# Kernel optimization log

Hardware: AMD Instinct MI355X
Metric: run time of the kernel (lower is better)

Reference implementation:

```python
import jax, jax.numpy as jnp
import numpy as np
import math

B, N, F, H = 16, 256, 1024, 16
HD = F // H  # head_dim = 64
NEG = -9e15


def setup_inputs() -> dict:
    key = jax.random.key(0)
    ks = jax.random.split(key, 12)
    s = 0.02
    return {
        "obj_feats": jax.random.normal(ks[0], (B, N, F), jnp.float32),
        "cross_feats": jax.random.normal(ks[1], (B, N, F), jnp.float32),
        "adj_matrix": jax.random.randint(ks[2], (B, N, N), 0, 2, jnp.int32),
        "label_biases_att": jax.random.normal(ks[3], (B, N, N), jnp.float32),
        "Wq": jax.random.normal(ks[4], (F, F), jnp.float32) * s,
        "bq": jnp.zeros((F,), jnp.float32),
        "Wk": jax.random.normal(ks[5], (F, F), jnp.float32) * s,
        "bk": jnp.zeros((F,), jnp.float32),
        "Wv": jax.random.normal(ks[6], (F, F), jnp.float32) * s,
        "bv": jnp.zeros((F,), jnp.float32),
        # grouped 1x1 conv: out=F, groups=H, in_per_group=F -> weight [F, F]
        "Wo": jax.random.normal(ks[7], (F, F), jnp.float32) * s,
        "bo": jnp.zeros((F,), jnp.float32),
    }


def reference(obj_feats, cross_feats, adj_matrix, label_biases_att,
              Wq, bq, Wk, bk, Wv, bv, Wo, bo):
    # projections (torch Linear: x @ W.T + b)
    q = (jnp.einsum('bnf,gf->bng', obj_feats, Wq) + bq).reshape(B, N, H, HD)
    k = (jnp.einsum('bnf,gf->bng', cross_feats, Wk) + bk).reshape(B, N, H, HD)
    v = jnp.einsum('bnf,gf->bng', cross_feats, Wv) + bv          # [B, N, F] (NOT split per head)

    scale = 1.0 / math.sqrt(float(HD))
    att = jnp.einsum('bqhd,bkhd->bqhk', q, k) * scale            # [B, Nq, H, Nk]

    # adjacency mask broadcast over heads + label bias (both indexed [b, q, k])
    mask = (adj_matrix > 0)[:, :, None, :]                       # [B, Nq, 1, Nk]
    att = jnp.where(mask, att, NEG) + label_biases_att[:, :, None, :]

    p = jax.nn.softmax(att, axis=-1)                             # softmax over keys

    # weighted sum against un-split values: [B, Nq, H, Nk] x [B, Nk, F]
    out = jnp.einsum('bqhk,bkf->bqhf', p, v)                     # [B, Nq, H, F]

    # grouped 1x1 conv: group h maps its F input channels -> HD output channels
    Wo_g = Wo.reshape(H, HD, F)
    out = jnp.einsum('bqhf,hdf->bqhd', out, Wo_g) + bo.reshape(H, HD)
    out = out.reshape(B, N, F)

    att_mean = p.sum(axis=2) / H                                 # [B, Nq, Nk]
    return out, att_mean
```

## Files before the change

### kernel.cpp

```cpp
#include <hip/hip_runtime.h>

#define NEGF -9e15f

typedef __attribute__((ext_vector_type(8))) unsigned short u16x8;
typedef __attribute__((ext_vector_type(8))) short          s16x8;
typedef __attribute__((ext_vector_type(4))) float          f32x4;

__device__ __forceinline__ unsigned short f2bf(float x) {
  union { float f; unsigned int u; } c; c.f = x;
  unsigned int r = c.u + 0x7fffu + ((c.u >> 16) & 1u);
  return (unsigned short)(r >> 16);
}
__device__ __forceinline__ float bf2f(unsigned short v) {
  union { float f; unsigned int u; } c; c.u = ((unsigned int)v) << 16;
  return c.f;
}

__device__ __forceinline__ void gload16(const void* g, void* l) {
  __builtin_amdgcn_global_load_lds(
      (const __attribute__((address_space(1))) unsigned int*)g,
      (__attribute__((address_space(3))) unsigned int*)l, 16, 0, 0);
}

__global__ __launch_bounds__(256) void cvt2_bf16(
    const float* __restrict__ a, const float* __restrict__ b,
    unsigned short* __restrict__ oa, unsigned short* __restrict__ ob)
{
  const int bid = blockIdx.x;
  const float* in = (bid < 4096) ? a : b;
  unsigned short* out = (bid < 4096) ? oa : ob;
  const int i = ((bid & 4095) * 256 + threadIdx.x) * 4;
  const float4 v = *(const float4*)(in + i);
  ushort4 o;
  o.x = f2bf(v.x); o.y = f2bf(v.y); o.z = f2bf(v.z); o.w = f2bf(v.w);
  *(ushort4*)(out + i) = o;
}

__global__ __launch_bounds__(256) void prep_w(
    const float* __restrict__ Wq, const float* __restrict__ Wk,
    const float* __restrict__ Wo, const float* __restrict__ Wv,
    unsigned short* __restrict__ Wall, unsigned short* __restrict__ Wo_bf,
    unsigned short* __restrict__ Wvt_bf)
{
  __shared__ float tile[32][33];
  const int bid = blockIdx.x;
  if (bid < 3072) {
    const int i = ((bid & 1023) * 256 + threadIdx.x) * 4;
    const float* in;
    unsigned short* out;
    float sc = 1.f;
    if (bid < 1024)      { in = Wq; out = Wall;           sc = 0.125f; }
    else if (bid < 2048) { in = Wk; out = Wall + 1048576; }
    else                 { in = Wo; out = Wo_bf; }
    const float4 v = *(const float4*)(in + i);
    ushort4 o;
    o.x = f2bf(v.x * sc); o.y = f2bf(v.y * sc);
    o.z = f2bf(v.z * sc); o.w = f2bf(v.w * sc);
    *(ushort4*)(out + i) = o;
  } else {
    const int j = bid - 3072;
    const int bc = (j & 31) * 32, br = (j >> 5) * 32;
    const int tx = threadIdx.x & 31, ty8 = threadIdx.x >> 5;
    #pragma unroll
    for (int jj = 0; jj < 32; jj += 8)
      tile[ty8 + jj][tx] = Wv[(size_t)(br + ty8 + jj) * 1024 + bc + tx];
    __syncthreads();
    #pragma unroll
    for (int jj = 0; jj < 32; jj += 8)
      Wvt_bf[(size_t)(bc + ty8 + jj) * 1024 + br + tx] = f2bf(tile[tx][ty8 + jj]);
  }
}

__global__ __launch_bounds__(256) void prep_bias(
    const float* __restrict__ bq, const float* __restrict__ bk,
    const float* __restrict__ Wo, const float* __restrict__ bv,
    float* __restrict__ ball)
{
  const int bid = blockIdx.x;
  if (bid < 4) {
    const int i = bid * 256 + threadIdx.x;
    ball[i]        = 0.125f * bq[i];
    ball[1024 + i] = bk[i];
  } else {
    const int g    = (bid - 4) * 4 + (threadIdx.x >> 6);
    const int lane = threadIdx.x & 63;
    float acc = 0.f;
    for (int f = lane; f < 1024; f += 64)
      acc = fmaf(Wo[(size_t)g * 1024 + f], bv[f], acc);
    #pragma unroll
    for (int off = 32; off > 0; off >>= 1) acc += __shfl_down(acc, off);
    if (lane == 0) ball[2048 + g] = acc;
  }
}

__global__ __launch_bounds__(256) void mb_prep(
    const int* __restrict__ adj, const float* __restrict__ lab,
    float* __restrict__ mb)
{
  const int i = (blockIdx.x * 256 + threadIdx.x) * 4;
  const int4   a = *(const int4*)(adj + i);
  const float4 l = *(const float4*)(lab + i);
  float4 o;
  o.x = a.x > 0 ? l.x : NEGF;
  o.y = a.y > 0 ? l.y : NEGF;
  o.z = a.z > 0 ? l.z : NEGF;
  o.w = a.w > 0 ? l.w : NEGF;
  *(float4*)(mb + i) = o;
}

__global__ __launch_bounds__(256, 3) void gemm_wov(
    const unsigned short* __restrict__ A,
    const unsigned short* __restrict__ Bw,
    unsigned short* __restrict__ Cout)
{
  __shared__ unsigned short Asm[128 * 64];
  __shared__ unsigned short Bsm[64 * 64];
  const int t = threadIdx.x;
  const int lane = t & 63, w = t >> 6;
  const int wm = w >> 1, wn = w & 1;
  const int bm = blockIdx.y * 128, bn = blockIdx.x * 64;

  const int srow = lane >> 3;
  const int skel = (lane & 7) * 8;
  const int fr = lane & 15, kf = (lane >> 4) * 8;

  f32x4 acc[4][2] = {};

  for (int k0 = 0; k0 < 1024; k0 += 64) {
    if (k0) __syncthreads();
    #pragma unroll
    for (int i = 0; i < 4; ++i) {
      const int c = i * 4 + w;
      const int r = c * 8 + srow;
      gload16(A + (size_t)(bm + r) * 1024 + k0 + skel, &Asm[c * 512]);
    }
    #pragma unroll
    for (int i = 0; i < 2; ++i) {
      const int c = i * 4 + w;
      const int r = c * 8 + srow;
      gload16(Bw + (size_t)(bn + r) * 1024 + k0 + skel, &Bsm[c * 512]);
    }
    __syncthreads();
    #pragma unroll
    for (int kk = 0; kk < 2; ++kk) {
      s16x8 af[4], bf[2];
      #pragma unroll
      for (int fm = 0; fm < 4; ++fm)
        af[fm] = *(const s16x8*)&Asm[(wm * 64 + fm * 16 + fr) * 64 + kk * 32 + kf];
      #pragma unroll
      for (int fn = 0; fn < 2; ++fn)
        bf[fn] = *(const s16x8*)&Bsm[(wn * 32 + fn * 16 + fr) * 64 + kk * 32 + kf];
      #pragma unroll
      for (int fm = 0; fm < 4; ++fm)
        #pragma unroll
        for (int fn = 0; fn < 2; ++fn)
          acc[fm][fn] = __builtin_amdgcn_mfma_f32_16x16x32_bf16(af[fm], bf[fn], acc[fm][fn], 0, 0, 0);
    }
  }

  const int rg = (lane >> 4) * 4;
  #pragma unroll
  for (int fm = 0; fm < 4; ++fm)
    #pragma unroll
    for (int fn = 0; fn < 2; ++fn) {
      const int col = bn + wn * 32 + fn * 16 + fr;
      #pragma unroll
      for (int r = 0; r < 4; ++r) {
        const int row = bm + wm * 64 + fm * 16 + rg + r;
        Cout[(size_t)row * 1024 + col] = f2bf(acc[fm][fn][r]);
      }
    }
}

__global__ __launch_bounds__(256, 3) void gemm_big(
    const unsigned short* __restrict__ objA,
    const unsigned short* __restrict__ crossA,
    const unsigned short* __restrict__ Wall,
    const float* __restrict__ ball,
    unsigned short* __restrict__ Qo,
    unsigned short* __restrict__ Ko,
    unsigned short* __restrict__ VWt)
{
  __shared__ unsigned short Asm[128 * 64];
  __shared__ unsigned short Bsm[128 * 64];
  const int t = threadIdx.x;
  const int w = t >> 6, lane = t & 63;
  const int wm = w >> 1, wn = w & 1;

  const int bid = blockIdx.x;
  const int xcd = bid & 7, j = bid >> 3;
  const int bmi = (xcd >> 1) * 8 + j / 12;
  const int bni = (xcd & 1) * 12 + j % 12;
  const int bm = bmi * 128;
  const int bn = bni * 128;
  const unsigned short* Ag = (bn < 1024) ? objA : crossA;

  const int srow = lane >> 3;
  const int skel = (lane & 7) * 8;
  const int fr = lane & 15, kf = (lane >> 4) * 8;

  f32x4 acc[4][4] = {};

  for (int k0 = 0; k0 < 1024; k0 += 64) {
    if (k0) __syncthreads();
    #pragma unroll
    for (int i = 0; i < 4; ++i) {
      const int c = i * 4 + w;
      const int r = c * 8 + srow;
      gload16(Ag   + (size_t)(bm + r) * 1024 + k0 + skel, &Asm[c * 512]);
      gload16(Wall + (size_t)(bn + r) * 1024 + k0 + skel, &Bsm[c * 512]);
    }
    __syncthreads();
    #pragma unroll
    for (int kk = 0; kk < 2; ++kk) {
      s16x8 af[4], bf[4];
      #pragma unroll
      for (int fm = 0; fm < 4; ++fm)
        af[fm] = *(const s16x8*)&Asm[(wm * 64 + fm * 16 + fr) * 64 + kk * 32 + kf];
      #pragma unroll
      for (int fn = 0; fn < 4; ++fn)
        bf[fn] = *(const s16x8*)&Bsm[(wn * 64 + fn * 16 + fr) * 64 + kk * 32 + kf];
      #pragma unroll
      for (int fm = 0; fm < 4; ++fm)
        #pragma unroll
        for (int fn = 0; fn < 4; ++fn)
          acc[fm][fn] = __builtin_amdgcn_mfma_f32_16x16x32_bf16(af[fm], bf[fn], acc[fm][fn], 0, 0, 0);
    }
  }

  const int rg = (lane >> 4) * 4;
  const int mode = bn >> 10;
  #pragma unroll
  for (int fm = 0; fm < 4; ++fm) {
    #pragma unroll
    for (int fn = 0; fn < 4; ++fn) {
      const int col  = bn + wn * 64 + fn * 16 + fr;
      const int cl   = col & 1023;
      const float bb = ball[col];
      const int row0 = bm + wm * 64 + fm * 16 + rg;
      if (mode == 0) {
        #pragma unroll
        for (int r = 0; r < 4; ++r)
          Qo[(size_t)(row0 + r) * 1024 + cl] = f2bf(acc[fm][fn][r] + bb);
      } else if (mode == 1) {
        #pragma unroll
        for (int r = 0; r < 4; ++r)
          Ko[(size_t)(row0 + r) * 1024 + cl] = f2bf(acc[fm][fn][r] + bb);
      } else {
        const int bidx = row0 >> 8, tok = row0 & 255;
        ushort4 u;
        u.x = f2bf(acc[fm][fn][0] + bb);
        u.y = f2bf(acc[fm][fn][1] + bb);
        u.z = f2bf(acc[fm][fn][2] + bb);
        u.w = f2bf(acc[fm][fn][3] + bb);
        *(ushort4*)(VWt + ((size_t)bidx * 1024 + cl) * 256 + tok) = u;
      }
    }
  }
}

__global__ __launch_bounds__(256, 2) void attn_mfma(
    const unsigned short* __restrict__ Qg,
    const unsigned short* __restrict__ Kg,
    const unsigned short* __restrict__ VWt,
    const float* __restrict__ mb,
    const float* __restrict__ bo,
    float* __restrict__ outp, unsigned short* __restrict__ Pb)
{
  const int t = threadIdx.x;
  const int w = t >> 6, lane = t & 63;
  const int fr = lane & 15, grp = lane >> 4;
  const int bid = blockIdx.x;
  const int xcd = bid & 7, i = bid >> 3;
  const int h   = i & 15;
  const int bqt = xcd * 8 + (i >> 4);
  const int b   = bqt >> 2;
  const int qt  = bqt & 3;
  const int q0 = qt * 64 + w * 16;

  __shared__ __align__(16) unsigned short Ks[256 * 64];
  __shared__ __align__(16) unsigned short VWs[64 * 256];

  {
    const unsigned short* kb = Kg + (size_t)(b * 256) * 1024 + h * 64;
    const int colb = (lane & 7) * 16;
    #pragma unroll
    for (int c = 0; c < 8; ++c) {
      const int row = c * 32 + w * 8 + (lane >> 3);
      const int sb  = colb ^ ((row & 7) << 4);
      gload16(kb + (size_t)row * 1024 + (sb >> 1), (char*)Ks + c * 4096 + w * 1024);
    }
  }
  {
    const unsigned short* vwb = VWt + (size_t)(b * 16 + h) * 16384;
    const int xb = (lane & 31) * 16;
    #pragma unroll
    for (int c = 0; c < 8; ++c) {
      const int row = c * 8 + w * 2 + (lane >> 5);
      const int sb  = xb ^ ((row & 7) << 4);
      gload16(vwb + row * 256 + (sb >> 1), (char*)VWs + c * 4096 + w * 1024);
    }
  }

  const unsigned short* qp = Qg + ((size_t)(b * 256 + q0 + fr)) * 1024 + h * 64 + grp * 8;
  const s16x8 qf0 = *(const s16x8*)qp;
  const s16x8 qf1 = *(const s16x8*)(qp + 32);

  __syncthreads();

  const float* mbp = mb + ((size_t)(b * 256 + q0 + fr)) * 256 + grp * 4;
  const int colA = (grp * 16) ^ ((fr & 7) << 4);

  f32x4 s[16];
  #pragma unroll
  for (int nf = 0; nf < 16; ++nf) s[nf] = (f32x4){0.f, 0.f, 0.f, 0.f};

  s16x8 kA[8], kB[8];
  float4 mA[4], mB[4];
  float mx = -3e38f;

#define LOADB(KF, MF, nb)                                                    \
  { _Pragma("unroll") for (int i2 = 0; i2 < 4; ++i2) {                       \
      const char* rp = (const char*)Ks + (((nb)*4 + i2) * 16 + fr) * 128;    \
      KF[2*i2]   = *(const s16x8*)(rp + colA);                               \
      KF[2*i2+1] = *(const s16x8*)(rp + (colA ^ 64));                        \
      MF[i2]     = *(const float4*)(mbp + ((nb)*4 + i2) * 16); } }
#define MFMAB(KF, nb)                                                        \
  { _Pragma("unroll") for (int i2 = 0; i2 < 4; ++i2) {                       \
      s[(nb)*4+i2] = __builtin_amdgcn_mfma_f32_16x16x32_bf16(KF[2*i2],   qf0, s[(nb)*4+i2], 0, 0, 0); \
      s[(nb)*4+i2] = __builtin_amdgcn_mfma_f32_16x16x32_bf16(KF[2*i2+1], qf1, s[(nb)*4+i2], 0, 0, 0); } }
#define MASKB(MF, nb)                                                        \
  { _Pragma("unroll") for (int i2 = 0; i2 < 4; ++i2) {                       \
      _Pragma("unroll") for (int r = 0; r < 4; ++r) {                        \
        const float m = ((const float*)&MF[i2])[r];                          \
        const float v = (m > -1e14f) ? s[(nb)*4+i2][r] + m : m;              \
        s[(nb)*4+i2][r] = v; mx = fmaxf(mx, v); } } }

  LOADB(kA, mA, 0); LOADB(kB, mB, 1); MFMAB(kA, 0);
  MASKB(mA, 0);     LOADB(kA, mA, 2); MFMAB(kB, 1);
  MASKB(mB, 1);     LOADB(kB, mB, 3); MFMAB(kA, 2);
  MASKB(mA, 2);     LOADB(kA, mA, 4); MFMAB(kB, 3);
  MASKB(mB, 3);     LOADB(kB, mB, 5); MFMAB(kA, 4);
  MASKB(mA, 4);     LOADB(kA, mA, 6); MFMAB(kB, 5);
  MASKB(mB, 5);     LOADB(kB, mB, 7); MFMAB(kA, 6);
  MASKB(mA, 6);     MFMAB(kB, 7);     MASKB(mB, 7);
#undef LOADB
#undef MFMAB
#undef MASKB

  mx = fmaxf(mx, __shfl_xor(mx, 16));
  mx = fmaxf(mx, __shfl_xor(mx, 32));
  float sm = 0.f;
  #pragma unroll
  for (int nf = 0; nf < 16; ++nf)
    #pragma unroll
    for (int r = 0; r < 4; ++r) {
      const float e = __expf(s[nf][r] - mx);
      s[nf][r] = e;
      sm += e;
    }
  sm += __shfl_xor(sm, 16);
  sm += __shfl_xor(sm, 32);
  const float inv = 1.f / sm;

  uint2 u2[16];
  #pragma unroll
  for (int nf = 0; nf < 16; ++nf) {
    const unsigned lo = (unsigned)f2bf(s[nf][0] * inv) | ((unsigned)f2bf(s[nf][1] * inv) << 16);
    const unsigned hi = (unsigned)f2bf(s[nf][2] * inv) | ((unsigned)f2bf(s[nf][3] * inv) << 16);
    u2[nf] = make_uint2(lo, hi);
  }

  unsigned short* prow = Pb + (((size_t)(b * 16 + h)) * 256 + q0 + fr) * 256 + grp * 4;
  #pragma unroll
  for (int nf = 0; nf < 16; ++nf)
    *(uint2*)(prow + nf * 16) = u2[nf];

  f32x4 o[4];
  #pragma unroll
  for (int nf = 0; nf < 4; ++nf) o[nf] = (f32x4){0.f, 0.f, 0.f, 0.f};
  const int srcA = fr + ((grp & 1) << 5);
  const int srcB = srcA + 16;
  const int swz  = (fr & 7) << 4;
  const bool hiSel = (grp & 2);
  #pragma unroll
  for (int ks = 0; ks < 8; ++ks) {
    const int aLx = __shfl((int)u2[2 * ks].x,     srcA, 64);
    const int aLy = __shfl((int)u2[2 * ks].y,     srcA, 64);
    const int bLx = __shfl((int)u2[2 * ks].x,     srcB, 64);
    const int bLy = __shfl((int)u2[2 * ks].y,     srcB, 64);
    const int aHx = __shfl((int)u2[2 * ks + 1].x, srcA, 64);
    const int aHy = __shfl((int)u2[2 * ks + 1].y, srcA, 64);
    const int bHx = __shfl((int)u2[2 * ks + 1].x, srcB, 64);
    const int bHy = __shfl((int)u2[2 * ks + 1].y, srcB, 64);
    union { int4 i; s16x8 v; } pf;
    pf.i = hiSel ? make_int4(aHx, aHy, bHx, bHy) : make_int4(aLx, aLy, bLx, bLy);
    const int cb = (ks * 64 + grp * 16) ^ swz;
    #pragma unroll
    for (int nf = 0; nf < 4; ++nf) {
      const s16x8 vf = *(const s16x8*)((const char*)VWs + (nf * 16 + fr) * 512 + cb);
      o[nf] = __builtin_amdgcn_mfma_f32_16x16x32_bf16(pf.v, vf, o[nf], 0, 0, 0);
    }
  }

  #pragma unroll
  for (int nf = 0; nf < 4; ++nf) {
    const float bb = bo[h * 64 + nf * 16 + fr];
    #pragma unroll
    for (int r = 0; r < 4; ++r)
      outp[((size_t)b * 256 + q0 + grp * 4 + r) * 1024 + h * 64 + nf * 16 + fr]
          = o[nf][r] + bb;
  }
}

__global__ __launch_bounds__(256) void attm_reduce(
    const unsigned short* __restrict__ Pb, float* __restrict__ attm)
{
  const size_t idx = (size_t)blockIdx.x * 256 + threadIdx.x;
  const int    k8  = (int)(idx & 31);
  const size_t bq  = idx >> 5;
  const int    b   = (int)(bq >> 8);
  const int    q   = (int)(bq & 255);
  float s[8] = {};
  const unsigned short* base = Pb + (size_t)b * 1048576 + (size_t)q * 256 + k8 * 8;
  #pragma unroll
  for (int hh = 0; hh < 16; ++hh) {
    const u16x8 p = *(const u16x8*)(base + (size_t)hh * 65536);
    #pragma unroll
    for (int j = 0; j < 8; ++j) s[j] += bf2f(p[j]);
  }
  float* dst = attm + bq * 256 + k8 * 8;
  float4 r0, r1;
  r0.x = s[0] * 0.0625f; r0.y = s[1] * 0.0625f; r0.z = s[2] * 0.0625f; r0.w = s[3] * 0.0625f;
  r1.x = s[4] * 0.0625f; r1.y = s[5] * 0.0625f; r1.z = s[6] * 0.0625f; r1.w = s[7] * 0.0625f;
  *(float4*)dst = r0;
  *(float4*)(dst + 4) = r1;
}

extern "C" void kernel_launch(void* const* d_in, const int* in_sizes, int n_in,
                              void* d_out, int out_size, void* d_ws, size_t ws_size,
                              hipStream_t stream)
{
  const float* obj   = (const float*)d_in[0];
  const float* cross = (const float*)d_in[1];
  const int*   adj   = (const int*)d_in[2];
  const float* lab   = (const float*)d_in[3];
  const float* Wq    = (const float*)d_in[4];
  const float* bq    = (const float*)d_in[5];
  const float* Wk    = (const float*)d_in[6];
  const float* bk    = (const float*)d_in[7];
  const float* Wv    = (const float*)d_in[8];
  const float* bv    = (const float*)d_in[9];
  const float* Wo    = (const float*)d_in[10];
  const float* bo    = (const float*)d_in[11];

  float* out  = (float*)d_out;
  float* attm = out + (size_t)16 * 256 * 1024;

  char* ws = (char*)d_ws;
  unsigned short* obj_bf   = (unsigned short*)(ws + 0);
  unsigned short* cross_bf = (unsigned short*)(ws + 8388608);
  unsigned short* Qbf      = (unsigned short*)(ws + 16777216);
  unsigned short* Kbf      = (unsigned short*)(ws + 25165824);
  unsigned short* VWt      = (unsigned short*)(ws + 33554432);
  unsigned short* Wall     = (unsigned short*)(ws + 41943040);
  unsigned short* Wo_bf    = (unsigned short*)(ws + 48234496);
  unsigned short* Wvt_bf   = (unsigned short*)(ws + 50331648);
  float*          ball     = (float*)(ws + 50331648);
  unsigned short* Pbuf     = (unsigned short*)(ws + 52432896);
  float*          mbuf     = (float*)obj_bf;

  cvt2_bf16<<<8192, 256, 0, stream>>>(obj, cross, obj_bf, cross_bf);
  prep_w<<<4096, 256, 0, stream>>>(Wq, Wk, Wo, Wv, Wall, Wo_bf, Wvt_bf);

  gemm_wov<<<dim3(16, 8), 256, 0, stream>>>(Wo_bf, Wvt_bf, Wall + 2097152);

  prep_bias<<<260, 256, 0, stream>>>(bq, bk, Wo, bv, ball);

  gemm_big<<<768, 256, 0, stream>>>(
      obj_bf, cross_bf, Wall, ball, Qbf, Kbf, VWt);

  mb_prep<<<1024, 256, 0, stream>>>(adj, lab, mbuf);

  attn_mfma<<<1024, 256, 0, stream>>>(
      Qbf, Kbf, VWt, mbuf, bo, out, Pbuf);
  attm_reduce<<<512, 256, 0, stream>>>(Pbuf, attm);
}
```

Measured before the change: 119.7 us.

## Retile projection GEMM to 256x256 blocks with double-buffered swizzled LDS

The main QKV projection GEMM moves from 128x128 tiles with 256 threads to 256x256 tiles with 512 threads (8 waves, 128x64 per wave). Each wave now does more MFMA work per LDS fragment it loads. Global-to-LDS loads are double-buffered in 128KB of shared memory with an XOR swizzle to avoid bank conflicts, and wait counts plus raw barriers let the next tile's loads overlap compute. The change also adds s_setprio around the MFMA blocks. The cost is only 192 blocks on the device, which may leave some CUs idle and increase tail effects, plus heavier register and LDS pressure.

```diff
diff --git a/kernel.cpp b/kernel.cpp
--- a/kernel.cpp
+++ b/kernel.cpp
@@ -172,7 +172,7 @@
     }
 }
 
-__global__ __launch_bounds__(256, 3) void gemm_big(
+__global__ __launch_bounds__(512, 2) void gemm_big(
     const unsigned short* __restrict__ objA,
     const unsigned short* __restrict__ crossA,
     const unsigned short* __restrict__ Wall,
@@ -181,63 +181,103 @@
     unsigned short* __restrict__ Ko,
     unsigned short* __restrict__ VWt)
 {
-  __shared__ unsigned short Asm[128 * 64];
-  __shared__ unsigned short Bsm[128 * 64];
+  __shared__ __align__(16) char smem[131072];
   const int t = threadIdx.x;
-  const int w = t >> 6, lane = t & 63;
-  const int wm = w >> 1, wn = w & 1;
+  const int wid = t >> 6, lane = t & 63;
+  const int wm = wid >> 2, wn = wid & 3;
+  const int fr = lane & 15, grp = lane >> 4;
 
   const int bid = blockIdx.x;
   const int xcd = bid & 7, j = bid >> 3;
-  const int bmi = (xcd >> 1) * 8 + j / 12;
-  const int bni = (xcd & 1) * 12 + j % 12;
-  const int bm = bmi * 128;
-  const int bn = bni * 128;
-  const unsigned short* Ag = (bn < 1024) ? objA : crossA;
-
-  const int srow = lane >> 3;
-  const int skel = (lane & 7) * 8;
-  const int fr = lane & 15, kf = (lane >> 4) * 8;
-
-  f32x4 acc[4][4] = {};
-
-  for (int k0 = 0; k0 < 1024; k0 += 64) {
-    if (k0) __syncthreads();
+  const int bmi = (xcd >> 1) * 4 + j / 6;
+  const int bni = (xcd & 1) * 6 + j % 6;
+  const int bm = bmi * 256, bn = bni * 256;
+  const unsigned short* Ag = ((bni < 4) ? objA : crossA) + (size_t)bm * 1024;
+  const unsigned short* Bg = Wall + (size_t)bn * 1024;
+
+  const int r8 = lane >> 3, cb = (lane & 7) * 16;
+
+  f32x4 acc[8][4] = {};
+
+  auto STAGE = [&](char* ldsbase, int k0) {
     #pragma unroll
     for (int i = 0; i < 4; ++i) {
-      const int c = i * 4 + w;
-      const int r = c * 8 + srow;
-      gload16(Ag   + (size_t)(bm + r) * 1024 + k0 + skel, &Asm[c * 512]);
-      gload16(Wall + (size_t)(bn + r) * 1024 + k0 + skel, &Bsm[c * 512]);
-    }
-    __syncthreads();
-    #pragma unroll
-    for (int kk = 0; kk < 2; ++kk) {
-      s16x8 af[4], bf[4];
-      #pragma unroll
-      for (int fm = 0; fm < 4; ++fm)
-        af[fm] = *(const s16x8*)&Asm[(wm * 64 + fm * 16 + fr) * 64 + kk * 32 + kf];
-      #pragma unroll
-      for (int fn = 0; fn < 4; ++fn)
-        bf[fn] = *(const s16x8*)&Bsm[(wn * 64 + fn * 16 + fr) * 64 + kk * 32 + kf];
-      #pragma unroll
-      for (int fm = 0; fm < 4; ++fm)
+      const int row = i * 64 + wid * 8 + r8;
+      const int sc  = cb ^ ((row & 7) << 4);
+      gload16((const char*)(Ag + (size_t)row * 1024 + k0) + sc,
+              ldsbase + i * 8192 + wid * 1024);
+      gload16((const char*)(Bg + (size_t)row * 1024 + k0) + sc,
+              ldsbase + 32768 + i * 8192 + wid * 1024);
+    }
+  };
+
+  auto COMPUTE = [&](const char* Ab) {
+    const char* Bb = Ab + 32768;
+    s16x8 bfr[4][2];
+    #pragma unroll
+    for (int fn = 0; fn < 4; ++fn)
+      #pragma unroll
+      for (int kk = 0; kk < 2; ++kk) {
+        const int row = wn * 64 + fn * 16 + fr;
+        bfr[fn][kk] = *(const s16x8*)(Bb + row * 128 + ((kk * 64 + grp * 16) ^ ((row & 7) << 4)));
+      }
+    #pragma unroll
+    for (int qm = 0; qm < 2; ++qm) {
+      s16x8 afr[4][2];
+      #pragma unroll
+      for (int fm2 = 0; fm2 < 4; ++fm2)
         #pragma unroll
-        for (int fn = 0; fn < 4; ++fn)
-          acc[fm][fn] = __builtin_amdgcn_mfma_f32_16x16x32_bf16(af[fm], bf[fn], acc[fm][fn], 0, 0, 0);
-    }
-  }
-
-  const int rg = (lane >> 4) * 4;
+        for (int kk = 0; kk < 2; ++kk) {
+          const int row = wm * 128 + (qm * 4 + fm2) * 16 + fr;
+          afr[fm2][kk] = *(const s16x8*)(Ab + row * 128 + ((kk * 64 + grp * 16) ^ ((row & 7) << 4)));
+        }
+      __builtin_amdgcn_s_setprio(1);
+      #pragma unroll
+      for (int fm2 = 0; fm2 < 4; ++fm2)
+        #pragma unroll
+        for (int fn = 0; fn < 4; ++fn) {
+          acc[qm * 4 + fm2][fn] = __builtin_amdgcn_mfma_f32_16x16x32_bf16(
+              afr[fm2][0], bfr[fn][0], acc[qm * 4 + fm2][fn], 0, 0, 0);
+          acc[qm * 4 + fm2][fn] = __builtin_amdgcn_mfma_f32_16x16x32_bf16(
+              afr[fm2][1], bfr[fn][1], acc[qm * 4 + fm2][fn], 0, 0, 0);
+        }
+      __builtin_amdgcn_s_setprio(0);
+    }
+  };
+
+  STAGE(smem, 0);
+  STAGE(smem + 65536, 64);
+
+  #pragma unroll 2
+  for (int kt = 0; kt < 14; ++kt) {
+    asm volatile("s_waitcnt vmcnt(8)" ::: "memory");
+    __builtin_amdgcn_s_barrier();
+    asm volatile("" ::: "memory");
+    COMPUTE(smem + (kt & 1) * 65536);
+    asm volatile("" ::: "memory");
+    __builtin_amdgcn_s_barrier();
+    asm volatile("" ::: "memory");
+    STAGE(smem + (kt & 1) * 65536, (kt + 2) * 64);
+  }
+  asm volatile("s_waitcnt vmcnt(8)" ::: "memory");
+  __builtin_amdgcn_s_barrier();
+  asm volatile("" ::: "memory");
+  COMPUTE(smem);
+  asm volatile("s_waitcnt vmcnt(0)" ::: "memory");
+  __builtin_amdgcn_s_barrier();
+  asm volatile("" ::: "memory");
+  COMPUTE(smem + 65536);
+
+  const int rg = grp * 4;
   const int mode = bn >> 10;
   #pragma unroll
-  for (int fm = 0; fm < 4; ++fm) {
+  for (int fm = 0; fm < 8; ++fm) {
     #pragma unroll
     for (int fn = 0; fn < 4; ++fn) {
       const int col  = bn + wn * 64 + fn * 16 + fr;
       const int cl   = col & 1023;
       const float bb = ball[col];
-      const int row0 = bm + wm * 64 + fm * 16 + rg;
+      const int row0 = bm + wm * 128 + fm * 16 + rg;
       if (mode == 0) {
         #pragma unroll
         for (int r = 0; r < 4; ++r)
@@ -395,10 +435,10 @@
     const int bHy = __shfl((int)u2[2 * ks + 1].y, srcB, 64);
     union { int4 i; s16x8 v; } pf;
     pf.i = hiSel ? make_int4(aHx, aHy, bHx, bHy) : make_int4(aLx, aLy, bLx, bLy);
-    const int cb = (ks * 64 + grp * 16) ^ swz;
+    const int cbv = (ks * 64 + grp * 16) ^ swz;
     #pragma unroll
     for (int nf = 0; nf < 4; ++nf) {
-      const s16x8 vf = *(const s16x8*)((const char*)VWs + (nf * 16 + fr) * 512 + cb);
+      const s16x8 vf = *(const s16x8*)((const char*)VWs + (nf * 16 + fr) * 512 + cbv);
       o[nf] = __builtin_amdgcn_mfma_f32_16x16x32_bf16(pf.v, vf, o[nf], 0, 0, 0);
     }
   }
@@ -477,7 +517,7 @@
 
   prep_bias<<<260, 256, 0, stream>>>(bq, bk, Wo, bv, ball);
 
-  gemm_big<<<768, 256, 0, stream>>>(
+  gemm_big<<<192, 512, 0, stream>>>(
       obj_bf, cross_bf, Wall, ball, Qbf, Kbf, VWt);
 
   mb_prep<<<1024, 256, 0, stream>>>(adj, lab, mbuf);
```

After: 120.5 us. No clear change (+0.7%).
